# Kernel optimization log

Hardware: AMD Instinct MI355X
Metric: run time of the kernel (lower is better)

Reference implementation:

```python
import jax, jax.numpy as jnp
import numpy as np

SCOPE = 63
STD = 2.0


def _mexican_hat(scope: int, std: float) -> np.ndarray:
    # Ricker wavelet sampled symmetrically around 0 (semlc weight_initialization.mexican_hat)
    x = np.arange(scope, dtype=np.float64) - scope // 2
    norm = 2.0 / (np.sqrt(3.0 * std) * np.pi ** 0.25)
    w = norm * (1.0 - (x / std) ** 2) * np.exp(-(x ** 2) / (2.0 * std ** 2))
    return w.astype(np.float32)


def setup_inputs() -> dict:
    key = jax.random.key(0)
    activations = jax.random.normal(key, (64, 64, 128, SCOPE), dtype=jnp.float32)
    inhibition_filter = jnp.asarray(_mexican_hat(SCOPE, STD))
    return {"activations": activations, "inhibition_filter": inhibition_filter}


def reference(activations, inhibition_filter):
    # kronecker delta: 1 at index 0, zeros elsewhere
    delta = jnp.zeros((SCOPE,), dtype=activations.dtype).at[0].set(1.0)
    # full (two-sided) 1D FFT along the last axis, complex divide, inverse FFT
    fa = jnp.fft.fft(activations, axis=-1)            # [N, C, H, scope] complex64
    ff = jnp.fft.fft(delta - inhibition_filter)       # [scope] complex64
    out = jnp.fft.ifft(fa / ff, axis=-1)
    # torch.irfft(..., onesided=False) returns the real part of the inverse transform
    return jnp.real(out)
```

## Files before the change

### kernel.cpp

```cpp
#include <hip/hip_runtime.h>
#include <hip/hip_bf16.h>

#define SCOPE 63
#define BT 256
#define RPB 64

typedef __attribute__((ext_vector_type(8))) __bf16 v8bf;
typedef __attribute__((ext_vector_type(4))) float f32x4;

#define GLL(gp, lp) __builtin_amdgcn_global_load_lds(                         \
    (const __attribute__((address_space(1))) void*)(gp),                      \
    (__attribute__((address_space(3))) void*)(lp), 16, 0, 0)

#define WS_BHI_OFF 256
#define WS_BLO_OFF 8448

__global__ void compute_inverse_filter(const float* __restrict__ f,
                                       float* __restrict__ ws) {
    __shared__ double cd[SCOPE];
    __shared__ double sd[SCOPE];
    __shared__ double hre[SCOPE];
    __shared__ double him[SCOPE];
    __shared__ float gsm[SCOPE];
    const double TWO_PI = 6.283185307179586476925286766559;
    int t = threadIdx.x;

    if (t < SCOPE) {
        double ang = -TWO_PI * (double)t / (double)SCOPE;
        cd[t] = cos(ang);
        sd[t] = sin(ang);
    }
    __syncthreads();

    if (t < SCOPE) {
        double re = 0.0, im = 0.0;
        for (int n = 0; n < SCOPE; ++n) {
            double x = (n == 0 ? 1.0 : 0.0) - (double)f[n];
            int m = (t * n) % SCOPE;
            re += x * cd[m];
            im += x * sd[m];
        }
        double d = re * re + im * im;
        hre[t] = re / d;
        him[t] = -im / d;
    }
    __syncthreads();

    if (t < SCOPE) {
        double acc = 0.0;
        for (int k = 0; k < SCOPE; ++k) {
            int m = (k * t) % SCOPE;
            acc += hre[k] * cd[m] + him[k] * sd[m];
        }
        float gv = (float)(acc / (double)SCOPE);
        ws[t] = gv;
        gsm[t] = gv;
    }
    __syncthreads();

    __bf16* Bhi = (__bf16*)((char*)ws + WS_BHI_OFF);
    __bf16* Blo = (__bf16*)((char*)ws + WS_BLO_OFF);
    for (int fidx = t; fidx < 4096; fidx += blockDim.x) {
        const int j  = fidx & 7;
        const int fl = (fidx >> 3) & 63;
        const int kt = (fidx >> 9) & 1;
        const int nt = fidx >> 10;
        const int k  = 8 * (fl >> 4) + j + 32 * kt;
        const int n  = 16 * nt + (fl & 15);
        float v = (k < SCOPE && n < SCOPE) ? gsm[(n - k + SCOPE) % SCOPE] : 0.0f;
        __bf16 h = (__bf16)v;
        Bhi[fidx] = h;
        Blo[fidx] = (__bf16)(v - (float)h);
    }
}

__global__ void __launch_bounds__(BT)
circ_conv_kernel(const float* __restrict__ A,
                 const float* __restrict__ WS,
                 float* __restrict__ O) {
    __shared__ __align__(16) unsigned char tile[16384 + 16];

    const int tid = threadIdx.x;
    const int w   = tid >> 6;
    const int l   = tid & 63;
    const int c   = l & 15;
    const int q   = l >> 4;

    const long long row0 = (long long)blockIdx.x * RPB;
    const float* __restrict__ src = A + row0 * SCOPE;
    float* __restrict__ dst       = O + row0 * SCOPE;

    const bool last = ((int)blockIdx.x == (int)gridDim.x - 1);

#pragma unroll
    for (int it = 0; it < 4; ++it) {
        const int i  = it * 256 + tid;
        const int r  = i >> 4;
        const int gl = i & 15;
        const int gk = gl ^ (r & 7);
        const bool oob = (gk == 15) && last && (r == 63);
        if (!oob)
            GLL(src + r * SCOPE + 4 * gk, tile + i * 16);
    }
    if (last && tid < 4) {
        const int r = 63, gl = 15 ^ (r & 7);
        float v = (tid < 3) ? src[r * SCOPE + 60 + tid] : 0.0f;
        *(float*)(tile + r * 256 + gl * 16 + tid * 4) = v;
    }

    const v8bf* BH = (const v8bf*)((const char*)WS + WS_BHI_OFF);
    const v8bf* BL = (const v8bf*)((const char*)WS + WS_BLO_OFF);
    v8bf bh[4][2], bl[4][2];
#pragma unroll
    for (int nt = 0; nt < 4; ++nt)
#pragma unroll
        for (int kt = 0; kt < 2; ++kt) {
            bh[nt][kt] = BH[(nt * 2 + kt) * 64 + l];
            bl[nt][kt] = BL[(nt * 2 + kt) * 64 + l];
        }

    __syncthreads();

    const int r  = 16 * w + c;
    const int rx = r & 7;
    v8bf ah[2], al[2];
#pragma unroll
    for (int kt = 0; kt < 2; ++kt) {
        const int fg0 = 8 * kt + 2 * q;
        float4 v0 = *(const float4*)(tile + r * 256 + ((fg0 ^ rx) << 4));
        float4 v1 = *(const float4*)(tile + r * 256 + (((fg0 + 1) ^ rx) << 4));
        float tmp[8] = {v0.x, v0.y, v0.z, v0.w, v1.x, v1.y, v1.z, v1.w};
#pragma unroll
        for (int j = 0; j < 8; ++j) {
            float v = tmp[j];
            __bf16 h = (__bf16)v;
            ah[kt][j] = h;
            al[kt][j] = (__bf16)(v - (float)h);
        }
    }

    float* cw = (float*)(tile + w * 4096);
#pragma unroll
    for (int nt = 0; nt < 4; ++nt) {
        f32x4 acc = {0.f, 0.f, 0.f, 0.f};
#pragma unroll
        for (int kt = 0; kt < 2; ++kt) {
            acc = __builtin_amdgcn_mfma_f32_16x16x32_bf16(ah[kt], bh[nt][kt], acc, 0, 0, 0);
            acc = __builtin_amdgcn_mfma_f32_16x16x32_bf16(ah[kt], bl[nt][kt], acc, 0, 0, 0);
            acc = __builtin_amdgcn_mfma_f32_16x16x32_bf16(al[kt], bh[nt][kt], acc, 0, 0, 0);
        }
        const int col = 16 * nt + c;
        if (col < SCOPE) {
            float* cp = cw + (4 * q) * SCOPE + col;
#pragma unroll
            for (int i = 0; i < 4; ++i)
                cp[i * SCOPE] = acc[i];
        }
    }

    float* wdst = dst + (long long)w * (16 * SCOPE);
#pragma unroll
    for (int it = 0; it < 4; ++it) {
        const int gidx = it * 64 + l;
        if (gidx < 252) {
            float4 v = *(const float4*)(tile + w * 4096 + gidx * 16);
            *(float4*)(wdst + gidx * 4) = v;
        }
    }
}

extern "C" void kernel_launch(void* const* d_in, const int* in_sizes, int n_in,
                              void* d_out, int out_size, void* d_ws, size_t ws_size,
                              hipStream_t stream) {
    const float* activations = (const float*)d_in[0];
    const float* filt        = (const float*)d_in[1];
    float* out               = (float*)d_out;
    float* ws                = (float*)d_ws;

    hipLaunchKernelGGL(compute_inverse_filter, dim3(1), dim3(BT), 0, stream,
                       filt, ws);

    const long long total = (long long)in_sizes[0];
    const long long rows  = total / SCOPE;
    const int blocks      = (int)(rows / RPB);

    hipLaunchKernelGGL(circ_conv_kernel, dim3(blocks), dim3(BT), 0,
                       stream, activations, ws, out);
}
```

Measured before the change: 57.67 us.

## Process four tiles per block with double-buffered LDS prefetch

Each block now handles four 64-row tiles instead of one. It uses two LDS buffers so the async global-to-LDS load of the next tile is issued before computing and storing the current one. This aims to overlap load latency with the MFMA and store work, and to load the filter B fragments into registers once per four tiles instead of once per tile. In exchange, the block count drops by four, LDS per block doubles, and each barrier still waits for outstanding loads, which limits how much actually overlaps.

```diff
diff --git a/kernel.cpp b/kernel.cpp
--- a/kernel.cpp
+++ b/kernel.cpp
@@ -3,7 +3,9 @@
 
 #define SCOPE 63
 #define BT 256
-#define RPB 64
+#define RPT 64
+#define TPB 4
+#define TILE_B 16384
 
 typedef __attribute__((ext_vector_type(8))) __bf16 v8bf;
 typedef __attribute__((ext_vector_type(4))) float f32x4;
@@ -74,11 +76,85 @@
     }
 }
 
+__device__ __forceinline__ void stage_tile(const float* __restrict__ srcRows,
+                                           unsigned char* buf, int tid,
+                                           bool lastTile) {
+#pragma unroll
+    for (int it = 0; it < 4; ++it) {
+        const int i  = it * 256 + tid;
+        const int r  = i >> 4;
+        const int gl = i & 15;
+        const int gk = gl ^ (r & 7);
+        const bool oob = lastTile && (r == 63) && (gk == 15);
+        if (!oob)
+            GLL(srcRows + r * SCOPE + 4 * gk, buf + i * 16);
+    }
+    if (lastTile && tid < 4) {
+        const int r = 63, gl = 15 ^ 7;
+        float v = (tid < 3) ? srcRows[r * SCOPE + 60 + tid] : 0.0f;
+        *(float*)(buf + r * 256 + gl * 16 + tid * 4) = v;
+    }
+}
+
+__device__ __forceinline__ void compute_store(unsigned char* buf,
+                                              float* __restrict__ dstRows,
+                                              int w, int l, int c, int q,
+                                              const v8bf (&bh)[4][2],
+                                              const v8bf (&bl)[4][2]) {
+    const int r  = 16 * w + c;
+    const int rx = r & 7;
+    v8bf ah[2], al[2];
+#pragma unroll
+    for (int kt = 0; kt < 2; ++kt) {
+        const int fg0 = 8 * kt + 2 * q;
+        float4 v0 = *(const float4*)(buf + r * 256 + ((fg0 ^ rx) << 4));
+        float4 v1 = *(const float4*)(buf + r * 256 + (((fg0 + 1) ^ rx) << 4));
+        float tmp[8] = {v0.x, v0.y, v0.z, v0.w, v1.x, v1.y, v1.z, v1.w};
+#pragma unroll
+        for (int j = 0; j < 8; ++j) {
+            float v = tmp[j];
+            __bf16 h = (__bf16)v;
+            ah[kt][j] = h;
+            al[kt][j] = (__bf16)(v - (float)h);
+        }
+    }
+
+    float* cw = (float*)(buf + w * 4096);
+#pragma unroll
+    for (int nt = 0; nt < 4; ++nt) {
+        f32x4 acc = {0.f, 0.f, 0.f, 0.f};
+#pragma unroll
+        for (int kt = 0; kt < 2; ++kt) {
+            acc = __builtin_amdgcn_mfma_f32_16x16x32_bf16(ah[kt], bh[nt][kt], acc, 0, 0, 0);
+            acc = __builtin_amdgcn_mfma_f32_16x16x32_bf16(ah[kt], bl[nt][kt], acc, 0, 0, 0);
+            acc = __builtin_amdgcn_mfma_f32_16x16x32_bf16(al[kt], bh[nt][kt], acc, 0, 0, 0);
+        }
+        const int col = 16 * nt + c;
+        if (col < SCOPE) {
+            float* cp = cw + (4 * q) * SCOPE + col;
+#pragma unroll
+            for (int i = 0; i < 4; ++i)
+                cp[i * SCOPE] = acc[i];
+        }
+    }
+
+    float* wdst = dstRows + (long long)w * (16 * SCOPE);
+#pragma unroll
+    for (int it = 0; it < 4; ++it) {
+        const int gidx = it * 64 + l;
+        if (gidx < 252) {
+            float4 v = *(const float4*)(buf + w * 4096 + gidx * 16);
+            *(float4*)(wdst + gidx * 4) = v;
+        }
+    }
+}
+
 __global__ void __launch_bounds__(BT)
 circ_conv_kernel(const float* __restrict__ A,
                  const float* __restrict__ WS,
                  float* __restrict__ O) {
-    __shared__ __align__(16) unsigned char tile[16384 + 16];
+    __shared__ __align__(16) unsigned char bufA[TILE_B + 16];
+    __shared__ __align__(16) unsigned char bufB[TILE_B + 16];
 
     const int tid = threadIdx.x;
     const int w   = tid >> 6;
@@ -86,27 +162,8 @@
     const int c   = l & 15;
     const int q   = l >> 4;
 
-    const long long row0 = (long long)blockIdx.x * RPB;
-    const float* __restrict__ src = A + row0 * SCOPE;
-    float* __restrict__ dst       = O + row0 * SCOPE;
-
-    const bool last = ((int)blockIdx.x == (int)gridDim.x - 1);
-
-#pragma unroll
-    for (int it = 0; it < 4; ++it) {
-        const int i  = it * 256 + tid;
-        const int r  = i >> 4;
-        const int gl = i & 15;
-        const int gk = gl ^ (r & 7);
-        const bool oob = (gk == 15) && last && (r == 63);
-        if (!oob)
-            GLL(src + r * SCOPE + 4 * gk, tile + i * 16);
-    }
-    if (last && tid < 4) {
-        const int r = 63, gl = 15 ^ (r & 7);
-        float v = (tid < 3) ? src[r * SCOPE + 60 + tid] : 0.0f;
-        *(float*)(tile + r * 256 + gl * 16 + tid * 4) = v;
-    }
+    const long long tile0 = (long long)blockIdx.x * TPB;
+    const long long lastT = (long long)gridDim.x * TPB - 1;
 
     const v8bf* BH = (const v8bf*)((const char*)WS + WS_BHI_OFF);
     const v8bf* BL = (const v8bf*)((const char*)WS + WS_BLO_OFF);
@@ -119,54 +176,30 @@
             bl[nt][kt] = BL[(nt * 2 + kt) * 64 + l];
         }
 
-    __syncthreads();
-
-    const int r  = 16 * w + c;
-    const int rx = r & 7;
-    v8bf ah[2], al[2];
-#pragma unroll
-    for (int kt = 0; kt < 2; ++kt) {
-        const int fg0 = 8 * kt + 2 * q;
-        float4 v0 = *(const float4*)(tile + r * 256 + ((fg0 ^ rx) << 4));
-        float4 v1 = *(const float4*)(tile + r * 256 + (((fg0 + 1) ^ rx) << 4));
-        float tmp[8] = {v0.x, v0.y, v0.z, v0.w, v1.x, v1.y, v1.z, v1.w};
-#pragma unroll
-        for (int j = 0; j < 8; ++j) {
-            float v = tmp[j];
-            __bf16 h = (__bf16)v;
-            ah[kt][j] = h;
-            al[kt][j] = (__bf16)(v - (float)h);
-        }
-    }
-
-    float* cw = (float*)(tile + w * 4096);
-#pragma unroll
-    for (int nt = 0; nt < 4; ++nt) {
-        f32x4 acc = {0.f, 0.f, 0.f, 0.f};
-#pragma unroll
-        for (int kt = 0; kt < 2; ++kt) {
-            acc = __builtin_amdgcn_mfma_f32_16x16x32_bf16(ah[kt], bh[nt][kt], acc, 0, 0, 0);
-            acc = __builtin_amdgcn_mfma_f32_16x16x32_bf16(ah[kt], bl[nt][kt], acc, 0, 0, 0);
-            acc = __builtin_amdgcn_mfma_f32_16x16x32_bf16(al[kt], bh[nt][kt], acc, 0, 0, 0);
-        }
-        const int col = 16 * nt + c;
-        if (col < SCOPE) {
-            float* cp = cw + (4 * q) * SCOPE + col;
-#pragma unroll
-            for (int i = 0; i < 4; ++i)
-                cp[i * SCOPE] = acc[i];
-        }
-    }
-
-    float* wdst = dst + (long long)w * (16 * SCOPE);
-#pragma unroll
-    for (int it = 0; it < 4; ++it) {
-        const int gidx = it * 64 + l;
-        if (gidx < 252) {
-            float4 v = *(const float4*)(tile + w * 4096 + gidx * 16);
-            *(float4*)(wdst + gidx * 4) = v;
-        }
-    }
+#define SRC(tt) (A + (tile0 + (tt)) * (long long)(RPT * SCOPE))
+#define DST(tt) (O + (tile0 + (tt)) * (long long)(RPT * SCOPE))
+#define ISLAST(tt) (tile0 + (tt) == lastT)
+
+    stage_tile(SRC(0), bufA, tid, ISLAST(0));
+    __syncthreads();
+
+    stage_tile(SRC(1), bufB, tid, ISLAST(1));
+    compute_store(bufA, DST(0), w, l, c, q, bh, bl);
+    __syncthreads();
+
+    stage_tile(SRC(2), bufA, tid, ISLAST(2));
+    compute_store(bufB, DST(1), w, l, c, q, bh, bl);
+    __syncthreads();
+
+    stage_tile(SRC(3), bufB, tid, ISLAST(3));
+    compute_store(bufA, DST(2), w, l, c, q, bh, bl);
+    __syncthreads();
+
+    compute_store(bufB, DST(3), w, l, c, q, bh, bl);
+
+#undef SRC
+#undef DST
+#undef ISLAST
 }
 
 extern "C" void kernel_launch(void* const* d_in, const int* in_sizes, int n_in,
@@ -182,7 +215,8 @@
 
     const long long total = (long long)in_sizes[0];
     const long long rows  = total / SCOPE;
-    const int blocks      = (int)(rows / RPB);
+    const long long tiles = rows / RPT;
+    const int blocks      = (int)(tiles / TPB);
 
     hipLaunchKernelGGL(circ_conv_kernel, dim3(blocks), dim3(BT), 0,
                        stream, activations, ws, out);
```

New measurement: 58.66 us. No clear change (+1.7%).
